# Kernel optimization log

Hardware: AMD Instinct MI355X
Metric: run time of the kernel (lower is better)

The kernel has to match this reference:

```python
import jax, jax.numpy as jnp
import numpy as np

M, NQ, NKV, DX, DT = 8, 1024, 1024, 512, 2
H, HD = 8, 64            # num_heads, head_dim
INNER = H * HD           # 512
KHID = 16                # kernel MLP hidden dim
SCALE = HD ** -0.5


def setup_inputs() -> dict:
    key = jax.random.key(0)
    ks = jax.random.split(key, 16)
    s = lambda fan_in: 1.0 / np.sqrt(fan_in)
    return {
        "xq": jax.random.normal(ks[0], (M, NQ, DX), jnp.float32),
        "xk": jax.random.normal(ks[1], (M, NKV, DX), jnp.float32),
        "xv": jax.random.normal(ks[2], (M, NKV, DX), jnp.float32),
        "tq": jax.random.normal(ks[3], (M, NQ, DT), jnp.float32),
        "tk": jax.random.normal(ks[4], (M, NKV, DT), jnp.float32),
        # attention projections (bias=False for q/k/v, Linear bias for out)
        "w_q": jax.random.normal(ks[5], (DX, INNER), jnp.float32) * s(DX),
        "w_k": jax.random.normal(ks[6], (DX, INNER), jnp.float32) * s(DX),
        "w_v": jax.random.normal(ks[7], (DX, INNER), jnp.float32) * s(DX),
        "w_out": jax.random.normal(ks[8], (INNER, DX), jnp.float32) * s(INNER),
        "b_out": jnp.zeros((DX,), jnp.float32),
        # kernel MLP: dt -> KHID -> H (per-head pairwise bias)
        "kw1": jax.random.normal(ks[9], (DT, KHID), jnp.float32) * s(DT),
        "kb1": jnp.zeros((KHID,), jnp.float32),
        "kw2": jax.random.normal(ks[10], (KHID, H), jnp.float32) * s(KHID),
        "kb2": jnp.zeros((H,), jnp.float32),
    }


def reference(xq, xk, xv, tq, tk, w_q, w_k, w_v, w_out, b_out, kw1, kb1, kw2, kb2):
    # pairwise differences of input locations: [m, nq, nkv, dt]
    diff = tq[:, :, None, :] - tk[:, None, :, :]
    # kernel MLP -> per-head bias, rearranged to [m, h, nq, nkv]
    hmid = jax.nn.relu(diff @ kw1 + kb1)          # [m, nq, nkv, KHID]
    dots = jnp.einsum('mqkc,ch->mhqk', hmid, kw2) + kb2[None, :, None, None]
    # token attention: standard scaled QK scores
    q = (xq @ w_q).reshape(M, NQ, H, HD)          # [m, nq, h, d]
    k = (xk @ w_k).reshape(M, NKV, H, HD)
    token_dots = jnp.einsum('mqhd,mkhd->mhqk', q, k) * SCALE
    dots = dots + token_dots
    attn = jax.nn.softmax(dots, axis=-1)          # softmax over keys
    v = (xv @ w_v).reshape(M, NKV, H, HD)
    out = jnp.einsum('mhqk,mkhd->mqhd', attn, v).reshape(M, NQ, INNER)
    return out @ w_out + b_out                    # [m, nq, dx]
```

## Files before the change

kernel.cpp:

```cpp
#include <hip/hip_runtime.h>


typedef unsigned short u16;
typedef unsigned int   u32;
typedef short bf8 __attribute__((ext_vector_type(8)));
typedef float f4  __attribute__((ext_vector_type(4)));
typedef _Float16 h2 __attribute__((ext_vector_type(2)));

#define Mb 8
#define SCALE 0.125f
#define NTOK 4194304

__device__ __forceinline__ u16 f2bf(float f) {
    union { float f; u32 u; } v; v.f = f;
    u32 r = v.u + 0x7fffu + ((v.u >> 16) & 1u);
    return (u16)(r >> 16);
}
__device__ __forceinline__ u32 pk2(float a, float b) {
    u32 r;
    asm("v_cvt_pk_bf16_f32 %0, %1, %2" : "=v"(r) : "v"(a), "v"(b));
    return r;
}
__device__ __forceinline__ void gl_lds16(const u16* g, u16* l) {
    __builtin_amdgcn_global_load_lds(
        (const __attribute__((address_space(1))) u32*)g,
        (__attribute__((address_space(3))) u32*)l, 16, 0, 0);
}
__device__ __forceinline__ h2 h2_of(u32 x) {
    union { u32 u; h2 h; } c; c.u = x; return c.h;
}
__device__ __forceinline__ u32 u_of(h2 x) {
    union { h2 h; u32 u; } c; c.h = x; return c.u;
}
__device__ __forceinline__ float dot2(h2 a, h2 b, float c) {
#if __has_builtin(__builtin_amdgcn_fdot2)
    return __builtin_amdgcn_fdot2(a, b, c, false);
#else
    return fmaf((float)a[0], (float)b[0], fmaf((float)a[1], (float)b[1], c));
#endif
}

struct PArgs {
    const float* xs[3];
    const float* ws[4];
    u16* dstA;
    u16* dstW;
};

__global__ __launch_bounds__(256) void prep(PArgs p) {
    __shared__ u16 tl[64][80];
    const int tid = threadIdx.x;
    const int b = blockIdx.x;
    if (b < 1536) {
        #pragma unroll
        for (int it = 0; it < 4; ++it) {
            const u32 u = (u32)b * 256u + (u32)tid + (u32)it * 393216u;
            const int arr = u >> 19;
            const size_t off = (size_t)(u & 524287u) * 8;
            const float* s = p.xs[arr];
            float4 a0 = *(const float4*)(s + off);
            float4 a1 = *(const float4*)(s + off + 4);
            uint4 v;
            v.x = pk2(a0.x, a0.y); v.y = pk2(a0.z, a0.w);
            v.z = pk2(a1.x, a1.y); v.w = pk2(a1.z, a1.w);
            *(uint4*)(p.dstA + (size_t)arr * NTOK + off) = v;
        }
    } else {
        const int bb = b - 1536;
        const int mat = bb >> 6, t = bb & 63;
        const int kt = t >> 3, nt = t & 7;
        const float* src = p.ws[mat] + (size_t)kt * 64 * 512 + (size_t)nt * 64;
        const int r0 = tid >> 4, c4 = (tid & 15) * 4;
        #pragma unroll
        for (int rr = 0; rr < 4; ++rr) {
            const int row = r0 + rr * 16;
            float4 a = *(const float4*)(src + (size_t)row * 512 + c4);
            tl[c4 + 0][row] = f2bf(a.x);
            tl[c4 + 1][row] = f2bf(a.y);
            tl[c4 + 2][row] = f2bf(a.z);
            tl[c4 + 3][row] = f2bf(a.w);
        }
        __syncthreads();
        u16* dst = p.dstW + (size_t)mat * 262144 + (size_t)nt * 64 * 512 + (size_t)kt * 64;
        #pragma unroll
        for (int i = 0; i < 2; ++i) {
            const int s2 = tid + i * 256;
            const int nrow = s2 >> 3, k8 = (s2 & 7) * 8;
            *(uint4*)(dst + (size_t)nrow * 512 + k8) = *(const uint4*)&tl[nrow][k8];
        }
    }
}

struct GArgs {
    const u16*   A[3];
    const u16*   W[3];
    void*        C[3];
    const float* bias;
    int          modeT[3];
    int          outf32;
};

__global__ __launch_bounds__(256) void gemm_mfma(GArgs g) {
    __shared__ u16 Xs[128][32];
    __shared__ u16 Ws[128][32];

    const int z   = blockIdx.z;
    const int tid = threadIdx.x;
    const int w = tid >> 6, lane = tid & 63, quad = lane >> 4, l16 = lane & 15;
    const int wm = w >> 1, wn = w & 1;
    const int bid = blockIdx.y * 4 + blockIdx.x;
    const int swz = ((bid & 7) << 5) | (bid >> 3);
    const int n0 = (swz & 3) * 128, t0 = (swz >> 2) * 128;
    const int trans = g.modeT[z];

    f4 acc[4][4];
    #pragma unroll
    for (int i = 0; i < 4; ++i)
        #pragma unroll
        for (int j = 0; j < 4; ++j) acc[i][j] = (f4)0.f;

    const int lrow  = lane >> 2;
    const int kslot = (lane & 3) ^ ((lane >> 3) & 3);
    u16* ldsX0 = &Xs[w * 32][0];
    u16* ldsX1 = &Xs[w * 32 + 16][0];
    u16* ldsW0 = &Ws[w * 32][0];
    u16* ldsW1 = &Ws[w * 32 + 16][0];
    const u16* gA0 = g.A[z] + (size_t)(t0 + w * 32 + lrow) * 512 + kslot * 8;
    const u16* gA1 = gA0 + 16 * 512;
    const u16* gW0 = g.W[z] + (size_t)(n0 + w * 32 + lrow) * 512 + kslot * 8;
    const u16* gW1 = gW0 + 16 * 512;

    const int rslot = (quad ^ ((l16 >> 1) & 3)) * 8;

    for (int kc = 0; kc < 512; kc += 32) {
        __syncthreads();
        gl_lds16(gA0 + kc, ldsX0);
        gl_lds16(gA1 + kc, ldsX1);
        gl_lds16(gW0 + kc, ldsW0);
        gl_lds16(gW1 + kc, ldsW1);
        __syncthreads();

        const u16* Abase = trans ? &Xs[0][0] : &Ws[0][0];
        const u16* Bbase = trans ? &Ws[0][0] : &Xs[0][0];
        const int arow = (trans ? wm : wn) * 64;
        const int brow = (trans ? wn : wm) * 64;
        bf8 af[4], bf[4];
        #pragma unroll
        for (int i = 0; i < 4; ++i)
            af[i] = *(const bf8*)(Abase + (arow + i * 16 + l16) * 32 + rslot);
        #pragma unroll
        for (int j = 0; j < 4; ++j)
            bf[j] = *(const bf8*)(Bbase + (brow + j * 16 + l16) * 32 + rslot);
        #pragma unroll
        for (int i = 0; i < 4; ++i)
            #pragma unroll
            for (int j = 0; j < 4; ++j)
                acc[i][j] = __builtin_amdgcn_mfma_f32_16x16x32_bf16(af[i], bf[j], acc[i][j], 0, 0, 0);
    }

    if (g.outf32) {
        float* Co = (float*)g.C[z];
        #pragma unroll
        for (int i = 0; i < 4; ++i) {
            const int nb = n0 + wn * 64 + i * 16 + quad * 4;
            float4 bv = *(const float4*)&g.bias[nb];
            #pragma unroll
            for (int j = 0; j < 4; ++j) {
                const int tok = t0 + wm * 64 + j * 16 + l16;
                float4 st;
                st.x = acc[i][j][0] + bv.x; st.y = acc[i][j][1] + bv.y;
                st.z = acc[i][j][2] + bv.z; st.w = acc[i][j][3] + bv.w;
                *(float4*)&Co[(size_t)tok * 512 + nb] = st;
            }
        }
    } else if (!trans) {
        u16* C = (u16*)g.C[z];
        #pragma unroll
        for (int i = 0; i < 4; ++i) {
            const int nb = n0 + wn * 64 + i * 16 + quad * 4;
            #pragma unroll
            for (int j = 0; j < 4; ++j) {
                const int tok = t0 + wm * 64 + j * 16 + l16;
                uint2 pw;
                pw.x = pk2(acc[i][j][0], acc[i][j][1]);
                pw.y = pk2(acc[i][j][2], acc[i][j][3]);
                *(uint2*)&C[(size_t)tok * 512 + nb] = pw;
            }
        }
    } else {
        u16* Vt = (u16*)g.C[z];
        #pragma unroll
        for (int i = 0; i < 4; ++i) {
            const int tokb = t0 + wm * 64 + i * 16 + quad * 4;
            const int mb = tokb >> 10, tb = tokb & 1023;
            #pragma unroll
            for (int j = 0; j < 4; ++j) {
                const int n = n0 + wn * 64 + j * 16 + l16;
                uint2 pw;
                pw.x = pk2(acc[i][j][0], acc[i][j][1]);
                pw.y = pk2(acc[i][j][2], acc[i][j][3]);
                *(uint2*)&Vt[(size_t)mb * 524288 + (size_t)n * 1024 + tb] = pw;
            }
        }
    }
}

__global__ __launch_bounds__(256) void attn_mfma(
    const u16* __restrict__ Q, const u16* __restrict__ K,
    const u16* __restrict__ Vt,
    const float* __restrict__ tqp, const float* __restrict__ tkp,
    const float* __restrict__ kw1, const float* __restrict__ kb1,
    const float* __restrict__ kw2,
    u16* __restrict__ O)
{
    __shared__ u16   sK[8][64][8];
    __shared__ u16   sV[8][64][8];
    __shared__ u32   sv2[8][68];
    __shared__ u16   sP[4][16][68];

    const int tid = threadIdx.x;
    const int w = tid >> 6, lane = tid & 63, quad = lane >> 4, l16 = lane & 15;
    const int qt = blockIdx.x, h = blockIdx.y, m = blockIdx.z;
    const int q0 = qt * 64;
    const size_t qtok = (size_t)m * 1024 + q0 + w * 16 + l16;

    bf8 qf[2];
    {
        const u16* qp = Q + qtok * 512 + h * 64 + quad * 8;
        qf[0] = *(const bf8*)qp;
        qf[1] = *(const bf8*)(qp + 32);
    }
    h2 u2[8], w2p[8];
    {
        const float t0v = tqp[qtok * 2], t1v = tqp[qtok * 2 + 1];
        #pragma unroll
        for (int cp = 0; cp < 8; ++cp) {
            const int c0 = 2 * cp, c1 = 2 * cp + 1;
            float ua = fmaf(t0v, kw1[c0], fmaf(t1v, kw1[16 + c0], kb1[c0]));
            float ub = fmaf(t0v, kw1[c1], fmaf(t1v, kw1[16 + c1], kb1[c1]));
            u2[cp][0]  = (_Float16)ua;            u2[cp][1]  = (_Float16)ub;
            w2p[cp][0] = (_Float16)kw2[c0 * 8 + h]; w2p[cp][1] = (_Float16)kw2[c1 * 8 + h];
        }
    }

    float mrun = -1e30f, lrun = 0.f;
    f4 o[4];
    #pragma unroll
    for (int d = 0; d < 4; ++d) o[d] = (f4)0.f;

    for (int kt = 0; kt < 16; ++kt) {
        const int k0 = kt * 64;
        __syncthreads();
        #pragma unroll
        for (int i = 0; i < 2; ++i) {
            const int s = tid + i * 256;
            const int seg = s >> 6, key = s & 63;
            const u16* kp = K + ((size_t)m * 1024 + k0 + key) * 512 + h * 64 + seg * 8;
            *(uint4*)&sK[seg][key][0] = *(const uint4*)kp;
        }
        #pragma unroll
        for (int i = 0; i < 2; ++i) {
            const int s = tid + i * 256;
            const int ks = s >> 6, d = s & 63;
            const u16* vp = Vt + (size_t)m * 524288 + (size_t)(h * 64 + d) * 1024 + k0 + ks * 8;
            *(uint4*)&sV[ks][d][0] = *(const uint4*)vp;
        }
        {
            const int cp = tid >> 5;
            const int k2 = (tid & 31) * 2;
            const float* tkq = tkp + ((size_t)m * 1024 + k0 + k2) * 2;
            float4 t = *(const float4*)tkq;
            const float w0a = kw1[2 * cp],     w1a = kw1[16 + 2 * cp];
            const float w0b = kw1[2 * cp + 1], w1b = kw1[16 + 2 * cp + 1];
            h2 p0, p1;
            p0[0] = (_Float16)fmaf(t.x, w0a, t.y * w1a);
            p0[1] = (_Float16)fmaf(t.x, w0b, t.y * w1b);
            p1[0] = (_Float16)fmaf(t.z, w0a, t.w * w1a);
            p1[1] = (_Float16)fmaf(t.z, w0b, t.w * w1b);
            uint2 pw; pw.x = u_of(p0); pw.y = u_of(p1);
            *(uint2*)&sv2[cp][k2] = pw;
        }
        __syncthreads();

        f4 s[4];
        #pragma unroll
        for (int msub = 0; msub < 4; ++msub) {
            bf8 kf0 = *(const bf8*)&sK[quad][msub * 16 + l16][0];
            bf8 kf1 = *(const bf8*)&sK[4 + quad][msub * 16 + l16][0];
            s[msub] = __builtin_amdgcn_mfma_f32_16x16x32_bf16(kf0, qf[0], (f4)0.f, 0, 0, 0);
            s[msub] = __builtin_amdgcn_mfma_f32_16x16x32_bf16(kf1, qf[1], s[msub], 0, 0, 0);
        }
        #pragma unroll
        for (int msub = 0; msub < 4; ++msub) {
            const int kb = msub * 16 + quad * 4;
            f4 b = (f4)0.f;
            #pragma unroll
            for (int cp = 0; cp < 8; ++cp) {
                uint4 vv = *(const uint4*)&sv2[cp][kb];
                const h2 uc = u2[cp], wc = w2p[cp];
                const h2 z = (h2)(_Float16)0.f;
                h2 d0 = uc - h2_of(vv.x);
                h2 d1 = uc - h2_of(vv.y);
                h2 d2 = uc - h2_of(vv.z);
                h2 d3 = uc - h2_of(vv.w);
                d0 = __builtin_elementwise_max(d0, z);
                d1 = __builtin_elementwise_max(d1, z);
                d2 = __builtin_elementwise_max(d2, z);
                d3 = __builtin_elementwise_max(d3, z);
                b[0] = dot2(d0, wc, b[0]);
                b[1] = dot2(d1, wc, b[1]);
                b[2] = dot2(d2, wc, b[2]);
                b[3] = dot2(d3, wc, b[3]);
            }
            s[msub] = s[msub] * SCALE + b;
        }
        float mx = -1e30f;
        #pragma unroll
        for (int msub = 0; msub < 4; ++msub) {
            mx = fmaxf(mx, fmaxf(fmaxf(s[msub][0], s[msub][1]),
                                 fmaxf(s[msub][2], s[msub][3])));
        }
        mx = fmaxf(mx, __shfl_xor(mx, 16));
        mx = fmaxf(mx, __shfl_xor(mx, 32));
        const float mnew = fmaxf(mrun, mx);
        float ps = 0.f;
        #pragma unroll
        for (int msub = 0; msub < 4; ++msub) {
            #pragma unroll
            for (int r = 0; r < 4; ++r) {
                float p = __expf(s[msub][r] - mnew);
                s[msub][r] = p;
                ps += p;
            }
        }
        ps += __shfl_xor(ps, 16);
        ps += __shfl_xor(ps, 32);
        if (__all(mx <= mrun)) {
            lrun += ps;
        } else {
            const float alpha = __expf(mrun - mnew);
            lrun = lrun * alpha + ps;
            mrun = mnew;
            #pragma unroll
            for (int d = 0; d < 4; ++d) o[d] = o[d] * alpha;
        }
        #pragma unroll
        for (int msub = 0; msub < 4; ++msub) {
            uint2 pw;
            pw.x = pk2(s[msub][0], s[msub][1]);
            pw.y = pk2(s[msub][2], s[msub][3]);
            *(uint2*)&sP[w][l16][msub * 16 + quad * 4] = pw;
        }
        #pragma unroll
        for (int dsub = 0; dsub < 4; ++dsub) {
            #pragma unroll
            for (int kc2 = 0; kc2 < 2; ++kc2) {
                bf8 vf = *(const bf8*)&sV[kc2 * 4 + quad][dsub * 16 + l16][0];
                bf8 pf = *(const bf8*)&sP[w][l16][kc2 * 32 + quad * 8];
                o[dsub] = __builtin_amdgcn_mfma_f32_16x16x32_bf16(vf, pf, o[dsub], 0, 0, 0);
            }
        }
    }

    const float inv = 1.f / lrun;
    #pragma unroll
    for (int dsub = 0; dsub < 4; ++dsub) {
        uint2 pw;
        pw.x = pk2(o[dsub][0] * inv, o[dsub][1] * inv);
        pw.y = pk2(o[dsub][2] * inv, o[dsub][3] * inv);
        *(uint2*)&O[qtok * 512 + h * 64 + dsub * 16 + quad * 4] = pw;
    }
}

extern "C" void kernel_launch(void* const* d_in, const int* in_sizes, int n_in,
                              void* d_out, int out_size, void* d_ws, size_t ws_size,
                              hipStream_t stream) {
    const float* xq    = (const float*)d_in[0];
    const float* xk    = (const float*)d_in[1];
    const float* xv    = (const float*)d_in[2];
    const float* tq    = (const float*)d_in[3];
    const float* tk    = (const float*)d_in[4];
    const float* w_q   = (const float*)d_in[5];
    const float* w_k   = (const float*)d_in[6];
    const float* w_v   = (const float*)d_in[7];
    const float* w_out = (const float*)d_in[8];
    const float* b_out = (const float*)d_in[9];
    const float* kw1   = (const float*)d_in[10];
    const float* kb1   = (const float*)d_in[11];
    const float* kw2   = (const float*)d_in[12];

    u16* Q  = (u16*)d_ws;
    u16* Kp = Q  + NTOK;
    u16* Vt = Kp + NTOK;
    u16* Aq = Vt + NTOK;
    u16* Ak = Aq + NTOK;
    u16* Av = Ak + NTOK;
    u16* Wq = Av + NTOK;
    u16* Wk = Wq + 262144;
    u16* Wv = Wk + 262144;
    u16* Wo = Wv + 262144;
    u16* O  = Aq;

    PArgs p;
    p.xs[0] = xq;  p.xs[1] = xk;  p.xs[2] = xv;
    p.ws[0] = w_q; p.ws[1] = w_k; p.ws[2] = w_v; p.ws[3] = w_out;
    p.dstA = Aq;   p.dstW = Wq;
    prep<<<dim3(1792), 256, 0, stream>>>(p);

    GArgs gq;
    gq.A[0] = Aq;  gq.A[1] = Ak;  gq.A[2] = Av;
    gq.W[0] = Wq;  gq.W[1] = Wk;  gq.W[2] = Wv;
    gq.C[0] = Q;   gq.C[1] = Kp;  gq.C[2] = Vt;
    gq.bias = nullptr;
    gq.modeT[0] = 0; gq.modeT[1] = 0; gq.modeT[2] = 1;
    gq.outf32 = 0;
    gemm_mfma<<<dim3(4, 64, 3), 256, 0, stream>>>(gq);

    attn_mfma<<<dim3(16, 8, Mb), 256, 0, stream>>>(Q, Kp, Vt, tq, tk,
                                                   kw1, kb1, kw2, O);

    GArgs go;
    go.A[0] = O;   go.A[1] = O;   go.A[2] = O;
    go.W[0] = Wo;  go.W[1] = Wo;  go.W[2] = Wo;
    go.C[0] = d_out; go.C[1] = d_out; go.C[2] = d_out;
    go.bias = b_out;
    go.modeT[0] = 0; go.modeT[1] = 0; go.modeT[2] = 0;
    go.outf32 = 1;
    gemm_mfma<<<dim3(4, 64, 1), 256, 0, stream>>>(go);
}
```

Measured before the change: 265.3 us.

## Double-buffer attention K/V tiles via async LDS loads with 128-query blocks

The attention kernel now uses 512-thread blocks covering 128 queries, so each K/V tile staged in LDS serves twice as many queries. K and V tiles, plus the per-key MLP term, are double-buffered: the next tile is loaded directly into LDS with global_load_lds while the current tile is computed, which cuts the two barriers per iteration to one. The aim is to hide global-load latency and halve K/V traffic per query. The cost is more LDS per block and half as many blocks (512), which could reduce occupancy and how well the grid fills the device.

```diff
diff --git a/kernel.cpp b/kernel.cpp
--- a/kernel.cpp
+++ b/kernel.cpp
@@ -205,7 +205,7 @@
     }
 }
 
-__global__ __launch_bounds__(256) void attn_mfma(
+__global__ __launch_bounds__(512) void attn_mfma(
     const u16* __restrict__ Q, const u16* __restrict__ K,
     const u16* __restrict__ Vt,
     const float* __restrict__ tqp, const float* __restrict__ tkp,
@@ -213,15 +213,15 @@
     const float* __restrict__ kw2,
     u16* __restrict__ O)
 {
-    __shared__ u16   sK[8][64][8];
-    __shared__ u16   sV[8][64][8];
-    __shared__ u32   sv2[8][68];
-    __shared__ u16   sP[4][16][68];
+    __shared__ u16 sK[2][8][64][8];
+    __shared__ u16 sV[2][8][64][8];
+    __shared__ u32 sv2[2][8][68];
+    __shared__ u16 sP[8][16][68];
 
     const int tid = threadIdx.x;
     const int w = tid >> 6, lane = tid & 63, quad = lane >> 4, l16 = lane & 15;
     const int qt = blockIdx.x, h = blockIdx.y, m = blockIdx.z;
-    const int q0 = qt * 64;
+    const int q0 = qt * 128;
     const size_t qtok = (size_t)m * 1024 + q0 + w * 16 + l16;
 
     bf8 qf[2];
@@ -238,55 +238,45 @@
             const int c0 = 2 * cp, c1 = 2 * cp + 1;
             float ua = fmaf(t0v, kw1[c0], fmaf(t1v, kw1[16 + c0], kb1[c0]));
             float ub = fmaf(t0v, kw1[c1], fmaf(t1v, kw1[16 + c1], kb1[c1]));
-            u2[cp][0]  = (_Float16)ua;            u2[cp][1]  = (_Float16)ub;
+            u2[cp][0]  = (_Float16)ua;              u2[cp][1]  = (_Float16)ub;
             w2p[cp][0] = (_Float16)kw2[c0 * 8 + h]; w2p[cp][1] = (_Float16)kw2[c1 * 8 + h];
         }
     }
+    const float w0a = kw1[2 * w],     w1a = kw1[16 + 2 * w];
+    const float w0b = kw1[2 * w + 1], w1b = kw1[16 + 2 * w + 1];
+
+    const u16* gK = K + ((size_t)m * 1024 + lane) * 512 + h * 64 + w * 8;
+    const u16* gV = Vt + (size_t)m * 524288 + (size_t)(h * 64 + lane) * 1024 + w * 8;
+    const float* gT = tkp + (size_t)m * 2048 + lane * 2;
 
     float mrun = -1e30f, lrun = 0.f;
     f4 o[4];
     #pragma unroll
     for (int d = 0; d < 4; ++d) o[d] = (f4)0.f;
 
+    auto STAGE = [&](int kt2, int nb) {
+        const int k0n = kt2 * 64;
+        float2 t = *(const float2*)(gT + k0n * 2);
+        h2 pv;
+        pv[0] = (_Float16)fmaf(t.x, w0a, t.y * w1a);
+        pv[1] = (_Float16)fmaf(t.x, w0b, t.y * w1b);
+        sv2[nb][w][lane] = u_of(pv);
+        gl_lds16(gK + (size_t)k0n * 512, &sK[nb][w][0][0]);
+        gl_lds16(gV + k0n,               &sV[nb][w][0][0]);
+    };
+
+    STAGE(0, 0);
+    __syncthreads();
+
+    int cur = 0;
     for (int kt = 0; kt < 16; ++kt) {
-        const int k0 = kt * 64;
-        __syncthreads();
-        #pragma unroll
-        for (int i = 0; i < 2; ++i) {
-            const int s = tid + i * 256;
-            const int seg = s >> 6, key = s & 63;
-            const u16* kp = K + ((size_t)m * 1024 + k0 + key) * 512 + h * 64 + seg * 8;
-            *(uint4*)&sK[seg][key][0] = *(const uint4*)kp;
-        }
-        #pragma unroll
-        for (int i = 0; i < 2; ++i) {
-            const int s = tid + i * 256;
-            const int ks = s >> 6, d = s & 63;
-            const u16* vp = Vt + (size_t)m * 524288 + (size_t)(h * 64 + d) * 1024 + k0 + ks * 8;
-            *(uint4*)&sV[ks][d][0] = *(const uint4*)vp;
-        }
-        {
-            const int cp = tid >> 5;
-            const int k2 = (tid & 31) * 2;
-            const float* tkq = tkp + ((size_t)m * 1024 + k0 + k2) * 2;
-            float4 t = *(const float4*)tkq;
-            const float w0a = kw1[2 * cp],     w1a = kw1[16 + 2 * cp];
-            const float w0b = kw1[2 * cp + 1], w1b = kw1[16 + 2 * cp + 1];
-            h2 p0, p1;
-            p0[0] = (_Float16)fmaf(t.x, w0a, t.y * w1a);
-            p0[1] = (_Float16)fmaf(t.x, w0b, t.y * w1b);
-            p1[0] = (_Float16)fmaf(t.z, w0a, t.w * w1a);
-            p1[1] = (_Float16)fmaf(t.z, w0b, t.w * w1b);
-            uint2 pw; pw.x = u_of(p0); pw.y = u_of(p1);
-            *(uint2*)&sv2[cp][k2] = pw;
-        }
-        __syncthreads();
+        if (kt < 15) STAGE(kt + 1, cur ^ 1);
 
         f4 s[4];
         #pragma unroll
         for (int msub = 0; msub < 4; ++msub) {
-            bf8 kf0 = *(const bf8*)&sK[quad][msub * 16 + l16][0];
-            bf8 kf1 = *(const bf8*)&sK[4 + quad][msub * 16 + l16][0];
+            bf8 kf0 = *(const bf8*)&sK[cur][quad][msub * 16 + l16][0];
+            bf8 kf1 = *(const bf8*)&sK[cur][4 + quad][msub * 16 + l16][0];
             s[msub] = __builtin_amdgcn_mfma_f32_16x16x32_bf16(kf0, qf[0], (f4)0.f, 0, 0, 0);
             s[msub] = __builtin_amdgcn_mfma_f32_16x16x32_bf16(kf1, qf[1], s[msub], 0, 0, 0);
         }
@@ -296,7 +286,7 @@
             f4 b = (f4)0.f;
             #pragma unroll
             for (int cp = 0; cp < 8; ++cp) {
-                uint4 vv = *(const uint4*)&sv2[cp][kb];
+                uint4 vv = *(const uint4*)&sv2[cur][cp][kb];
                 const h2 uc = u2[cp], wc = w2p[cp];
                 const h2 z = (h2)(_Float16)0.f;
                 h2 d0 = uc - h2_of(vv.x);
@@ -355,11 +345,14 @@
         for (int dsub = 0; dsub < 4; ++dsub) {
             #pragma unroll
             for (int kc2 = 0; kc2 < 2; ++kc2) {
-                bf8 vf = *(const bf8*)&sV[kc2 * 4 + quad][dsub * 16 + l16][0];
+                bf8 vf = *(const bf8*)&sV[cur][kc2 * 4 + quad][dsub * 16 + l16][0];
                 bf8 pf = *(const bf8*)&sP[w][l16][kc2 * 32 + quad * 8];
                 o[dsub] = __builtin_amdgcn_mfma_f32_16x16x32_bf16(vf, pf, o[dsub], 0, 0, 0);
             }
         }
+
+        if (kt < 15) __syncthreads();
+        cur ^= 1;
     }
 
     const float inv = 1.f / lrun;
@@ -416,8 +409,8 @@
     gq.outf32 = 0;
     gemm_mfma<<<dim3(4, 64, 3), 256, 0, stream>>>(gq);
 
-    attn_mfma<<<dim3(16, 8, Mb), 256, 0, stream>>>(Q, Kp, Vt, tq, tk,
-                                                   kw1, kb1, kw2, O);
+    attn_mfma<<<dim3(8, 8, Mb), 512, 0, stream>>>(Q, Kp, Vt, tq, tk,
+                                                  kw1, kb1, kw2, O);
 
     GArgs go;
     go.A[0] = O;   go.A[1] = O;   go.A[2] = O;
```

Result: faster. 246.9 us (-6.9%).
